# Performance work log

Hardware: AMD Instinct MI355X
Metric: run time of the kernel (lower is better)

## Reference

```python
import jax, jax.numpy as jnp
import numpy as np

N_NODES = 100000
N_EDGES = 3200000
N_FEAT = 128
EMBED = 20
N_CLASSES = 10
N_GRAPHS = 64


def setup_inputs() -> dict:
    key = jax.random.key(0)
    ks = jax.random.split(key, 8)
    x = jax.random.normal(ks[0], (N_NODES, N_FEAT), dtype=jnp.float32)
    edge_index = jax.random.randint(ks[1], (2, N_EDGES), 0, N_NODES, dtype=jnp.int64)
    edge_weights = jax.random.uniform(ks[2], (N_EDGES,), dtype=jnp.float32)
    batch = jnp.sort(jax.random.randint(ks[3], (N_NODES,), 0, N_GRAPHS, dtype=jnp.int64))
    # GCNConv parameters (glorot-ish scale) and final linear layer
    W = jax.random.normal(ks[4], (N_FEAT, EMBED), dtype=jnp.float32) * (1.0 / np.sqrt(N_FEAT))
    b = jnp.zeros((EMBED,), dtype=jnp.float32)
    lin_W = jax.random.normal(ks[5], (2 * EMBED, N_CLASSES), dtype=jnp.float32) * (1.0 / np.sqrt(2 * EMBED))
    lin_b = jnp.zeros((N_CLASSES,), dtype=jnp.float32)
    return {"x": x, "edge_index": edge_index, "edge_weights": edge_weights,
            "batch": batch, "W": W, "b": b, "lin_W": lin_W, "lin_b": lin_b}


def reference(x, edge_index, edge_weights, batch, W, b, lin_W, lin_b):
    N = x.shape[0]
    # --- GCNConv with self-loops and symmetric normalization (PyG semantics) ---
    loops = jnp.arange(N, dtype=edge_index.dtype)
    src = jnp.concatenate([edge_index[0], loops])
    dst = jnp.concatenate([edge_index[1], loops])
    w = jnp.concatenate([edge_weights, jnp.ones((N,), dtype=edge_weights.dtype)])
    deg = jax.ops.segment_sum(w, dst, num_segments=N)  # degree at targets
    dinv = jnp.where(deg > 0, jax.lax.rsqrt(deg), 0.0)
    norm = dinv[src] * w * dinv[dst]  # [E+N]
    xw = x @ W  # [N, EMBED]
    msg = xw[src] * norm[:, None]  # gather + scale
    out1 = jax.ops.segment_sum(msg, dst, num_segments=N) + b  # scatter-add
    # --- L2 normalize per node (F.normalize p=2 dim=1, eps=1e-12), then ReLU ---
    nrm = jnp.sqrt(jnp.sum(out1 * out1, axis=1, keepdims=True))
    embed = jax.nn.relu(out1 / jnp.maximum(nrm, 1e-12))
    # --- global max / mean pool per graph ---
    mx = jax.ops.segment_max(embed, batch, num_segments=N_GRAPHS)
    mx = jnp.where(jnp.isfinite(mx), mx, 0.0)  # empty graphs -> 0
    cnt = jax.ops.segment_sum(jnp.ones((N,), dtype=embed.dtype), batch, num_segments=N_GRAPHS)
    mean = jax.ops.segment_sum(embed, batch, num_segments=N_GRAPHS) / jnp.maximum(cnt, 1.0)[:, None]
    pooled = jnp.concatenate([mx, mean], axis=-1)  # [G, 2*EMBED]
    return pooled @ lin_W + lin_b
```

## Files before the change

### kernel.cpp

```cpp
#include <hip/hip_runtime.h>
#include <hip/hip_fp16.h>

#define NN 100000
#define NE 3200000
#define NF 128
#define EM 20
#define NC 10
#define NG 64

#define NB 782
#define CAPB 4608
#define T 4096
#define SBLK 1024

__global__ __launch_bounds__(SBLK) void k_scatter(
        const int* __restrict__ src, const int* __restrict__ dst,
        const float* __restrict__ w, int* __restrict__ gcursor,
        uint2* __restrict__ barr) {
    __shared__ unsigned int cnt[1024];
    __shared__ unsigned int off[1024];
    __shared__ unsigned int gbase[NB];
    __shared__ unsigned int wsum[16];
    __shared__ uint2 staged[T];
    __shared__ unsigned short bkt[T];
    int tid = threadIdx.x;
    long E0 = (long)blockIdx.x * T;
    int tot = (int)min((long)T, (long)NE - E0);
    cnt[tid] = 0;
    __syncthreads();
    unsigned int dreg[T / SBLK];
#pragma unroll
    for (int k = 0; k < T / SBLK; ++k) {
        int e = k * SBLK + tid;
        dreg[k] = 0;
        if (e < tot) {
            dreg[k] = (unsigned)dst[E0 + e];
            atomicAdd(&cnt[dreg[k] >> 7], 1u);
        }
    }
    __syncthreads();
    {
        int lane = tid & 63, wv = tid >> 6;
        unsigned int v = cnt[tid];
        unsigned int s = v;
#pragma unroll
        for (int o = 1; o < 64; o <<= 1) {
            unsigned int t = __shfl_up(s, o);
            if (lane >= o) s += t;
        }
        if (lane == 63) wsum[wv] = s;
        __syncthreads();
        if (tid == 0) {
            unsigned int a = 0;
#pragma unroll
            for (int i = 0; i < 16; ++i) { unsigned int t = wsum[i]; wsum[i] = a; a += t; }
        }
        __syncthreads();
        off[tid] = wsum[wv] + s - v;
    }
    __syncthreads();
    if (tid < NB) {
        unsigned int c = cnt[tid];
        gbase[tid] = c ? (unsigned int)atomicAdd(&gcursor[tid], (int)c) : 0u;
        cnt[tid] = 0;
    }
    __syncthreads();
#pragma unroll
    for (int k = 0; k < T / SBLK; ++k) {
        int e = k * SBLK + tid;
        if (e < tot) {
            long ge = E0 + e;
            unsigned int d = dreg[k];
            unsigned int b = d >> 7;
            unsigned int slot = atomicAdd(&cnt[b], 1u);
            unsigned int pos = off[b] + slot;
            staged[pos] = make_uint2((((unsigned)src[ge]) << 7) | (d & 127u),
                                     __float_as_uint(w[ge]));
            bkt[pos] = (unsigned short)b;
        }
    }
    __syncthreads();
    for (int i = tid; i < tot; i += SBLK) {
        unsigned int b = bkt[i];
        unsigned int gpos = gbase[b] + ((unsigned)i - off[b]);
        if (gpos < CAPB) barr[(size_t)b * CAPB + gpos] = staged[i];
    }
}

__global__ void k_degb(const int* __restrict__ gcursor, const uint2* __restrict__ barr,
                       float* __restrict__ dinv) {
    __shared__ float dacc[128];
    int bk = blockIdx.x, tid = threadIdx.x;
    if (tid < 128) dacc[tid] = 0.f;
    __syncthreads();
    int cntb = min(gcursor[bk], CAPB);
    const uint2* row = barr + (size_t)bk * CAPB;
    for (int i = tid; i < cntb; i += 1024) {
        uint2 r = row[i];
        atomicAdd(&dacc[r.x & 127u], __uint_as_float(r.y));
    }
    __syncthreads();
    if (tid < 128) {
        int gd = bk * 128 + tid;
        if (gd < NN) dinv[gd] = rsqrtf(1.0f + dacc[tid]);
    }
}

__global__ void k_xw(const float* __restrict__ x, const float* __restrict__ W,
                     const float* __restrict__ dinv,
                     __half* __restrict__ xwhA, __half* __restrict__ xwhB) {
    __shared__ float xs[64 * 129];
    __shared__ float Ws[NF * EM];
    int base = blockIdx.x * 64;
    for (int i = threadIdx.x; i < NF * EM; i += 256) Ws[i] = W[i];
    const float4* xg = (const float4*)(x + (size_t)base * NF);
    for (int v = threadIdx.x; v < 64 * NF / 4; v += 256) {
        int fidx = v * 4;
        size_t gidx = (size_t)base * NF + fidx;
        float4 val = (gidx + 3 < (size_t)NN * NF) ? xg[v] : make_float4(0.f, 0.f, 0.f, 0.f);
        int r = fidx / NF, c = fidx % NF;
        float* p = xs + r * 129 + c;
        p[0] = val.x; p[1] = val.y; p[2] = val.z; p[3] = val.w;
    }
    __syncthreads();
    int n = threadIdx.x & 63;
    int jg = threadIdx.x >> 6;
    int j0 = jg * 5;
    if (base + n >= NN) return;
    float acc[5] = {0.f, 0.f, 0.f, 0.f, 0.f};
    const float* xr = xs + n * 129;
#pragma unroll 4
    for (int k = 0; k < NF; ++k) {
        float xv = xr[k];
        const float* wr = Ws + k * EM + j0;
#pragma unroll
        for (int jj = 0; jj < 5; ++jj) acc[jj] = fmaf(xv, wr[jj], acc[jj]);
    }
    float dv = dinv[base + n];
#pragma unroll
    for (int jj = 0; jj < 5; ++jj) {
        int j = j0 + jj;
        __half hv = __float2half(acc[jj] * dv);
        if (j < 16) xwhA[(size_t)(base + n) * 16 + j] = hv;
        else        xwhB[(size_t)(base + n) * 4 + (j - 16)] = hv;
    }
}

__device__ inline void unpack16(uint4 a0, uint4 a1, float* f) {
    const __half2* h = (const __half2*)&a0;
#pragma unroll
    for (int c = 0; c < 4; ++c) { float2 t = __half22float2(h[c]); f[2*c] = t.x; f[2*c+1] = t.y; }
    h = (const __half2*)&a1;
#pragma unroll
    for (int c = 0; c < 4; ++c) { float2 t = __half22float2(h[c]); f[8+2*c] = t.x; f[9+2*c] = t.y; }
}
__device__ inline void unpack4(uint2 b0, float* f) {
    const __half2* h = (const __half2*)&b0;
#pragma unroll
    for (int c = 0; c < 2; ++c) { float2 t = __half22float2(h[c]); f[2*c] = t.x; f[2*c+1] = t.y; }
}

__global__ __launch_bounds__(1024, 8) void k_sortaggr(
                           const int* __restrict__ gcursor,
                           const unsigned long long* __restrict__ barr64,
                           const __half* __restrict__ xwhA, const __half* __restrict__ xwhB,
                           const float* __restrict__ dinv, const float* __restrict__ b,
                           float* __restrict__ embed) {
    __shared__ unsigned long long srt[CAPB];
    __shared__ unsigned int cnt[128];
    __shared__ unsigned int off[128];
    __shared__ unsigned int wtot;
    int bk = blockIdx.x, tid = threadIdx.x;
    if (tid < 128) cnt[tid] = 0;
    __syncthreads();
    int cntb = min(gcursor[bk], CAPB);
    const unsigned long long* row = barr64 + (size_t)bk * CAPB;
    unsigned long long rec[5];
    unsigned int pos[5];
    int K = 0;
    for (int e = tid; e < cntb; e += 1024) {
        rec[K] = row[e];
        pos[K] = atomicAdd(&cnt[(unsigned)rec[K] & 127u], 1u);
        ++K;
    }
    __syncthreads();
    unsigned int v = 0, s = 0;
    if (tid < 128) {
        v = cnt[tid]; s = v;
#pragma unroll
        for (int o = 1; o < 64; o <<= 1) {
            unsigned int t = __shfl_up(s, o);
            if ((tid & 63) >= o) s += t;
        }
        if (tid == 63) wtot = s;
    }
    __syncthreads();
    if (tid < 128) {
        if (tid >= 64) s += wtot;
        off[tid] = s;
    }
    __syncthreads();
    for (int k = 0; k < K; ++k) {
        unsigned int dl = (unsigned)rec[k] & 127u;
        srt[off[dl] - cnt[dl] + pos[k]] = rec[k];
    }
    __syncthreads();
    int d = tid >> 3, sub = tid & 7;
    int s0 = (int)(off[d] - cnt[d]), s1 = (int)off[d];
    const uint4* pA = (const uint4*)xwhA;
    const uint2* pB = (const uint2*)xwhB;
    float acc[20];
#pragma unroll
    for (int j = 0; j < 20; ++j) acc[j] = 0.f;
    for (int e = s0 + sub; e < s1; e += 8) {
        unsigned long long r = srt[e];
        unsigned int sN = ((unsigned int)r) >> 7;
        float nw = __uint_as_float((unsigned int)(r >> 32));
        uint4 a0 = pA[(size_t)sN * 2];
        uint4 a1 = pA[(size_t)sN * 2 + 1];
        uint2 b0 = pB[sN];
        const __half2* h0 = (const __half2*)&a0;
#pragma unroll
        for (int c = 0; c < 4; ++c) {
            float2 t = __half22float2(h0[c]);
            acc[2*c]   = fmaf(t.x, nw, acc[2*c]);
            acc[2*c+1] = fmaf(t.y, nw, acc[2*c+1]);
        }
        const __half2* h1 = (const __half2*)&a1;
#pragma unroll
        for (int c = 0; c < 4; ++c) {
            float2 t = __half22float2(h1[c]);
            acc[8+2*c]   = fmaf(t.x, nw, acc[8+2*c]);
            acc[9+2*c]   = fmaf(t.y, nw, acc[9+2*c]);
        }
        const __half2* h2 = (const __half2*)&b0;
#pragma unroll
        for (int c = 0; c < 2; ++c) {
            float2 t = __half22float2(h2[c]);
            acc[16+2*c] = fmaf(t.x, nw, acc[16+2*c]);
            acc[17+2*c] = fmaf(t.y, nw, acc[17+2*c]);
        }
    }
#pragma unroll
    for (int j = 0; j < 20; ++j) {
        acc[j] += __shfl_xor(acc[j], 1);
        acc[j] += __shfl_xor(acc[j], 2);
        acc[j] += __shfl_xor(acc[j], 4);
    }
    if (sub == 0) {
        int gd = bk * 128 + d;
        if (gd < NN) {
            float dv = dinv[gd];
            uint4 a0 = pA[(size_t)gd * 2];
            uint4 a1 = pA[(size_t)gd * 2 + 1];
            uint2 b0 = pB[gd];
            float xdh[20];
            unpack16(a0, a1, xdh);
            unpack4(b0, xdh + 16);
            float ss = 0.f;
#pragma unroll
            for (int j = 0; j < 20; ++j) {
                float r = fmaf(dv, acc[j] + xdh[j], b[j]);
                acc[j] = r;
                ss = fmaf(r, r, ss);
            }
            float inv = 1.0f / fmaxf(sqrtf(ss), 1e-12f);
            float4 o4[5];
            float* o = (float*)o4;
#pragma unroll
            for (int j = 0; j < 20; ++j) {
                float e2 = acc[j] * inv;
                o[j] = e2 > 0.f ? e2 : 0.f;
            }
            float4* eo = (float4*)(embed + (size_t)gd * EM);
#pragma unroll
            for (int c = 0; c < 5; ++c) eo[c] = o4[c];
        }
    }
}

__device__ inline int lbound(const int* __restrict__ batch, int key) {
    int lo = 0, hi = NN;
    while (lo < hi) {
        int mid = (lo + hi) >> 1;
        if (batch[mid] < key) lo = mid + 1; else hi = mid;
    }
    return lo;
}

__global__ void k_poolfinal(const float* __restrict__ embed, const int* __restrict__ batch,
                            const float* __restrict__ lw, const float* __restrict__ lb,
                            float* __restrict__ out) {
    __shared__ float cross[4][40];
    __shared__ float pooled[40];
    int g = blockIdx.x;
    int s0 = lbound(batch, g), s1 = lbound(batch, g + 1);
    int cnt = s1 - s0;
    float mx[EM], sm[EM];
#pragma unroll
    for (int j = 0; j < EM; ++j) { mx[j] = 0.f; sm[j] = 0.f; }
    for (int n = s0 + threadIdx.x; n < s1; n += 256) {
        const float4* e = (const float4*)(embed + (size_t)n * EM);
#pragma unroll
        for (int c = 0; c < 5; ++c) {
            float4 v = e[c];
            int j = c * 4;
            mx[j+0] = fmaxf(mx[j+0], v.x); sm[j+0] += v.x;
            mx[j+1] = fmaxf(mx[j+1], v.y); sm[j+1] += v.y;
            mx[j+2] = fmaxf(mx[j+2], v.z); sm[j+2] += v.z;
            mx[j+3] = fmaxf(mx[j+3], v.w); sm[j+3] += v.w;
        }
    }
#pragma unroll
    for (int o = 32; o > 0; o >>= 1) {
#pragma unroll
        for (int j = 0; j < EM; ++j) {
            mx[j] = fmaxf(mx[j], __shfl_xor(mx[j], o));
            sm[j] += __shfl_xor(sm[j], o);
        }
    }
    int wave = threadIdx.x >> 6, lane = threadIdx.x & 63;
    if (lane == 0) {
#pragma unroll
        for (int j = 0; j < EM; ++j) { cross[wave][j] = mx[j]; cross[wave][EM + j] = sm[j]; }
    }
    __syncthreads();
    if (threadIdx.x < 40) {
        int j = threadIdx.x;
        float v = cross[0][j];
        if (j < EM) v = fmaxf(fmaxf(v, cross[1][j]), fmaxf(cross[2][j], cross[3][j]));
        else        v = v + cross[1][j] + cross[2][j] + cross[3][j];
        if (j >= EM) v *= 1.0f / fmaxf((float)cnt, 1.0f);
        pooled[j] = v;
    }
    __syncthreads();
    if (threadIdx.x < NC) {
        int c = threadIdx.x;
        float acc = lb[c];
#pragma unroll
        for (int j = 0; j < 2 * EM; ++j) acc = fmaf(pooled[j], lw[j * NC + c], acc);
        out[g * NC + c] = acc;
    }
}

static inline size_t align_up(size_t v) { return (v + 1023) & ~(size_t)1023; }

extern "C" void kernel_launch(void* const* d_in, const int* in_sizes, int n_in,
                              void* d_out, int out_size, void* d_ws, size_t ws_size,
                              hipStream_t stream) {
    const float* x     = (const float*)d_in[0];
    const int*   ei    = (const int*)d_in[1];
    const float* ew    = (const float*)d_in[2];
    const int*   batch = (const int*)d_in[3];
    const float* W     = (const float*)d_in[4];
    const float* b     = (const float*)d_in[5];
    const float* lw    = (const float*)d_in[6];
    const float* lb    = (const float*)d_in[7];
    float* out = (float*)d_out;

    char* ws = (char*)d_ws;
    int*    gcursor = (int*)ws;    ws += align_up(4096);
    float*  dinv    = (float*)ws;  ws += align_up((size_t)NN * 4);
    __half* xwhA    = (__half*)ws; ws += align_up((size_t)NN * 16 * 2);
    __half* xwhB    = (__half*)ws; ws += align_up((size_t)NN * 4 * 2);
    float*  embed   = (float*)ws;  ws += align_up((size_t)NN * EM * 4);
    uint2*  barr    = (uint2*)ws;
    unsigned long long* barr64 = (unsigned long long*)barr;

    const int* srcp = ei;
    const int* dstp = ei + NE;

    (void)hipMemsetAsync(gcursor, 0, 4096, stream);
    k_scatter<<<(NE + T - 1) / T, SBLK, 0, stream>>>(srcp, dstp, ew, gcursor, barr);
    k_degb<<<NB, 1024, 0, stream>>>(gcursor, barr, dinv);
    k_xw<<<(NN + 63) / 64, 256, 0, stream>>>(x, W, dinv, xwhA, xwhB);
    k_sortaggr<<<NB, 1024, 0, stream>>>(gcursor, barr64, xwhA, xwhB, dinv, b, embed);
    k_poolfinal<<<NG, 256, 0, stream>>>(embed, batch, lw, lb, out);
}
```

Before: 276.1 us.

## Halve aggregation block size and software-pipeline neighbor gathers two deep

The sort-and-aggregate kernel now runs with 512 threads per block, giving each destination node 4 lanes instead of 8, so each thread holds up to 9 records. The edge loop is software-pipelined so the gathers for the next two edges are issued before the FMAs of the current one, keeping more memory requests in flight per thread. This targets gather latency in the aggregation step. In exchange there is more register pressure and less thread-level parallelism per block, and the out-of-range prefetch reads node 0 when a destination has fewer edges.

```diff
diff --git a/kernel.cpp b/kernel.cpp
--- a/kernel.cpp
+++ b/kernel.cpp
@@ -160,7 +160,31 @@
     for (int c = 0; c < 2; ++c) { float2 t = __half22float2(h[c]); f[2*c] = t.x; f[2*c+1] = t.y; }
 }
 
-__global__ __launch_bounds__(1024, 8) void k_sortaggr(
+__device__ inline void fma20(float* acc, uint4 a0, uint4 a1, uint2 b0, float nw) {
+    const __half2* h0 = (const __half2*)&a0;
+#pragma unroll
+    for (int c = 0; c < 4; ++c) {
+        float2 t = __half22float2(h0[c]);
+        acc[2*c]   = fmaf(t.x, nw, acc[2*c]);
+        acc[2*c+1] = fmaf(t.y, nw, acc[2*c+1]);
+    }
+    const __half2* h1 = (const __half2*)&a1;
+#pragma unroll
+    for (int c = 0; c < 4; ++c) {
+        float2 t = __half22float2(h1[c]);
+        acc[8+2*c] = fmaf(t.x, nw, acc[8+2*c]);
+        acc[9+2*c] = fmaf(t.y, nw, acc[9+2*c]);
+    }
+    const __half2* h2 = (const __half2*)&b0;
+#pragma unroll
+    for (int c = 0; c < 2; ++c) {
+        float2 t = __half22float2(h2[c]);
+        acc[16+2*c] = fmaf(t.x, nw, acc[16+2*c]);
+        acc[17+2*c] = fmaf(t.y, nw, acc[17+2*c]);
+    }
+}
+
+__global__ __launch_bounds__(512) void k_sortaggr(
                            const int* __restrict__ gcursor,
                            const unsigned long long* __restrict__ barr64,
                            const __half* __restrict__ xwhA, const __half* __restrict__ xwhB,
@@ -175,10 +199,10 @@
     __syncthreads();
     int cntb = min(gcursor[bk], CAPB);
     const unsigned long long* row = barr64 + (size_t)bk * CAPB;
-    unsigned long long rec[5];
-    unsigned int pos[5];
+    unsigned long long rec[9];
+    unsigned int pos[9];
     int K = 0;
-    for (int e = tid; e < cntb; e += 1024) {
+    for (int e = tid; e < cntb; e += 512) {
         rec[K] = row[e];
         pos[K] = atomicAdd(&cnt[(unsigned)rec[K] & 127u], 1u);
         ++K;
@@ -205,47 +229,47 @@
         srt[off[dl] - cnt[dl] + pos[k]] = rec[k];
     }
     __syncthreads();
-    int d = tid >> 3, sub = tid & 7;
+    int d = tid >> 2, sub = tid & 3;
     int s0 = (int)(off[d] - cnt[d]), s1 = (int)off[d];
     const uint4* pA = (const uint4*)xwhA;
     const uint2* pB = (const uint2*)xwhB;
     float acc[20];
 #pragma unroll
     for (int j = 0; j < 20; ++j) acc[j] = 0.f;
-    for (int e = s0 + sub; e < s1; e += 8) {
-        unsigned long long r = srt[e];
-        unsigned int sN = ((unsigned int)r) >> 7;
-        float nw = __uint_as_float((unsigned int)(r >> 32));
-        uint4 a0 = pA[(size_t)sN * 2];
-        uint4 a1 = pA[(size_t)sN * 2 + 1];
-        uint2 b0 = pB[sN];
-        const __half2* h0 = (const __half2*)&a0;
-#pragma unroll
-        for (int c = 0; c < 4; ++c) {
-            float2 t = __half22float2(h0[c]);
-            acc[2*c]   = fmaf(t.x, nw, acc[2*c]);
-            acc[2*c+1] = fmaf(t.y, nw, acc[2*c+1]);
-        }
-        const __half2* h1 = (const __half2*)&a1;
-#pragma unroll
-        for (int c = 0; c < 4; ++c) {
-            float2 t = __half22float2(h1[c]);
-            acc[8+2*c]   = fmaf(t.x, nw, acc[8+2*c]);
-            acc[9+2*c]   = fmaf(t.y, nw, acc[9+2*c]);
-        }
-        const __half2* h2 = (const __half2*)&b0;
-#pragma unroll
-        for (int c = 0; c < 2; ++c) {
-            float2 t = __half22float2(h2[c]);
-            acc[16+2*c] = fmaf(t.x, nw, acc[16+2*c]);
-            acc[17+2*c] = fmaf(t.y, nw, acc[17+2*c]);
-        }
+    int e0 = s0 + sub;
+    if (e0 < s1) {
+        unsigned long long rA = srt[e0];
+        unsigned int sA = ((unsigned int)rA) >> 7;
+        float nA = __uint_as_float((unsigned int)(rA >> 32));
+        uint4 A0 = pA[(size_t)sA * 2];
+        uint4 A1 = pA[(size_t)sA * 2 + 1];
+        uint2 A2 = pB[sA];
+        int eB = e0 + 4;
+        bool hB = eB < s1;
+        unsigned long long rB = hB ? srt[eB] : 0ULL;
+        unsigned int sB = ((unsigned int)rB) >> 7;
+        float nB = __uint_as_float((unsigned int)(rB >> 32));
+        uint4 B0 = pA[(size_t)sB * 2];
+        uint4 B1 = pA[(size_t)sB * 2 + 1];
+        uint2 B2 = pB[sB];
+        for (int ec = e0 + 8; ec < s1; ec += 4) {
+            unsigned long long rC = srt[ec];
+            unsigned int sC = ((unsigned int)rC) >> 7;
+            float nC = __uint_as_float((unsigned int)(rC >> 32));
+            uint4 C0 = pA[(size_t)sC * 2];
+            uint4 C1 = pA[(size_t)sC * 2 + 1];
+            uint2 C2 = pB[sC];
+            fma20(acc, A0, A1, A2, nA);
+            A0 = B0; A1 = B1; A2 = B2; nA = nB;
+            B0 = C0; B1 = C1; B2 = C2; nB = nC;
+        }
+        fma20(acc, A0, A1, A2, nA);
+        if (hB) fma20(acc, B0, B1, B2, nB);
     }
 #pragma unroll
     for (int j = 0; j < 20; ++j) {
         acc[j] += __shfl_xor(acc[j], 1);
         acc[j] += __shfl_xor(acc[j], 2);
-        acc[j] += __shfl_xor(acc[j], 4);
     }
     if (sub == 0) {
         int gd = bk * 128 + d;
@@ -374,6 +398,6 @@
     k_scatter<<<(NE + T - 1) / T, SBLK, 0, stream>>>(srcp, dstp, ew, gcursor, barr);
     k_degb<<<NB, 1024, 0, stream>>>(gcursor, barr, dinv);
     k_xw<<<(NN + 63) / 64, 256, 0, stream>>>(x, W, dinv, xwhA, xwhB);
-    k_sortaggr<<<NB, 1024, 0, stream>>>(gcursor, barr64, xwhA, xwhB, dinv, b, embed);
+    k_sortaggr<<<NB, 512, 0, stream>>>(gcursor, barr64, xwhA, xwhB, dinv, b, embed);
     k_poolfinal<<<NG, 256, 0, stream>>>(embed, batch, lw, lb, out);
 }
```

New measurement: 266.6 us. 3.4% less time.

## Fuse degree and fp16 projection scaling into aggregation kernel via grid barrier

Applied to the files above, without the earlier changes.

Removes the separate degree kernel and computes per-node degree inside the sort-aggregate kernel, which already reads each destination bucket, so the bucket array is no longer read twice. The node projection kernel now runs first and writes unscaled fp32 values; the fused kernel scales its own 128 nodes by the inverse square root of degree, writes the fp16 gather tables, then waits on a software grid-wide barrier (atomic counter plus spin) before gathering neighbours. Block size drops to 512 threads with 4 lanes per destination node, and the embed buffer now aliases the fp32 projection buffer. The barrier is only safe if all 782 blocks are resident at once, which carries deadlock risk, and the extra fp32 write and read adds memory traffic.

```diff
diff --git a/kernel.cpp b/kernel.cpp
--- a/kernel.cpp
+++ b/kernel.cpp
@@ -87,28 +87,8 @@
     }
 }
 
-__global__ void k_degb(const int* __restrict__ gcursor, const uint2* __restrict__ barr,
-                       float* __restrict__ dinv) {
-    __shared__ float dacc[128];
-    int bk = blockIdx.x, tid = threadIdx.x;
-    if (tid < 128) dacc[tid] = 0.f;
-    __syncthreads();
-    int cntb = min(gcursor[bk], CAPB);
-    const uint2* row = barr + (size_t)bk * CAPB;
-    for (int i = tid; i < cntb; i += 1024) {
-        uint2 r = row[i];
-        atomicAdd(&dacc[r.x & 127u], __uint_as_float(r.y));
-    }
-    __syncthreads();
-    if (tid < 128) {
-        int gd = bk * 128 + tid;
-        if (gd < NN) dinv[gd] = rsqrtf(1.0f + dacc[tid]);
-    }
-}
-
 __global__ void k_xw(const float* __restrict__ x, const float* __restrict__ W,
-                     const float* __restrict__ dinv,
-                     __half* __restrict__ xwhA, __half* __restrict__ xwhB) {
+                     float* __restrict__ xwf) {
     __shared__ float xs[64 * 129];
     __shared__ float Ws[NF * EM];
     int base = blockIdx.x * 64;
@@ -136,14 +116,9 @@
 #pragma unroll
         for (int jj = 0; jj < 5; ++jj) acc[jj] = fmaf(xv, wr[jj], acc[jj]);
     }
-    float dv = dinv[base + n];
-#pragma unroll
-    for (int jj = 0; jj < 5; ++jj) {
-        int j = j0 + jj;
-        __half hv = __float2half(acc[jj] * dv);
-        if (j < 16) xwhA[(size_t)(base + n) * 16 + j] = hv;
-        else        xwhB[(size_t)(base + n) * 4 + (j - 16)] = hv;
-    }
+#pragma unroll
+    for (int jj = 0; jj < 5; ++jj)
+        xwf[(size_t)(base + n) * EM + j0 + jj] = acc[jj];
 }
 
 __device__ inline void unpack16(uint4 a0, uint4 a1, float* f) {
@@ -160,27 +135,55 @@
     for (int c = 0; c < 2; ++c) { float2 t = __half22float2(h[c]); f[2*c] = t.x; f[2*c+1] = t.y; }
 }
 
-__global__ __launch_bounds__(1024, 8) void k_sortaggr(
-                           const int* __restrict__ gcursor,
+__device__ inline void fma20(float* acc, uint4 a0, uint4 a1, uint2 b0, float nw) {
+    const __half2* h0 = (const __half2*)&a0;
+#pragma unroll
+    for (int c = 0; c < 4; ++c) {
+        float2 t = __half22float2(h0[c]);
+        acc[2*c]   = fmaf(t.x, nw, acc[2*c]);
+        acc[2*c+1] = fmaf(t.y, nw, acc[2*c+1]);
+    }
+    const __half2* h1 = (const __half2*)&a1;
+#pragma unroll
+    for (int c = 0; c < 4; ++c) {
+        float2 t = __half22float2(h1[c]);
+        acc[8+2*c] = fmaf(t.x, nw, acc[8+2*c]);
+        acc[9+2*c] = fmaf(t.y, nw, acc[9+2*c]);
+    }
+    const __half2* h2 = (const __half2*)&b0;
+#pragma unroll
+    for (int c = 0; c < 2; ++c) {
+        float2 t = __half22float2(h2[c]);
+        acc[16+2*c] = fmaf(t.x, nw, acc[16+2*c]);
+        acc[17+2*c] = fmaf(t.y, nw, acc[17+2*c]);
+    }
+}
+
+__global__ __launch_bounds__(512, 8) void k_fused(
+                           const int* __restrict__ gcursor, int* bar,
                            const unsigned long long* __restrict__ barr64,
-                           const __half* __restrict__ xwhA, const __half* __restrict__ xwhB,
-                           const float* __restrict__ dinv, const float* __restrict__ b,
-                           float* __restrict__ embed) {
+                           const float* xwf,
+                           __half* __restrict__ xwhA, __half* __restrict__ xwhB,
+                           const float* __restrict__ b, float* embed) {
     __shared__ unsigned long long srt[CAPB];
     __shared__ unsigned int cnt[128];
     __shared__ unsigned int off[128];
+    __shared__ float dacc[128];
+    __shared__ float dvs[128];
     __shared__ unsigned int wtot;
     int bk = blockIdx.x, tid = threadIdx.x;
-    if (tid < 128) cnt[tid] = 0;
+    if (tid < 128) { cnt[tid] = 0; dacc[tid] = 0.f; }
     __syncthreads();
     int cntb = min(gcursor[bk], CAPB);
     const unsigned long long* row = barr64 + (size_t)bk * CAPB;
-    unsigned long long rec[5];
-    unsigned int pos[5];
+    unsigned long long rec[9];
+    unsigned int pos[9];
     int K = 0;
-    for (int e = tid; e < cntb; e += 1024) {
+    for (int e = tid; e < cntb; e += 512) {
         rec[K] = row[e];
-        pos[K] = atomicAdd(&cnt[(unsigned)rec[K] & 127u], 1u);
+        unsigned int dl = (unsigned)rec[K] & 127u;
+        pos[K] = atomicAdd(&cnt[dl], 1u);
+        atomicAdd(&dacc[dl], __uint_as_float((unsigned)(rec[K] >> 32)));
         ++K;
     }
     __syncthreads();
@@ -198,59 +201,54 @@
     if (tid < 128) {
         if (tid >= 64) s += wtot;
         off[tid] = s;
+        dvs[tid] = rsqrtf(1.0f + dacc[tid]);
     }
     __syncthreads();
     for (int k = 0; k < K; ++k) {
         unsigned int dl = (unsigned)rec[k] & 127u;
         srt[off[dl] - cnt[dl] + pos[k]] = rec[k];
     }
-    __syncthreads();
-    int d = tid >> 3, sub = tid & 7;
+    for (int i = tid; i < 128 * EM; i += 512) {
+        int node = i / EM, dim = i - node * EM;
+        int gd = bk * 128 + node;
+        if (gd < NN) {
+            __half hv = __float2half(xwf[(size_t)gd * EM + dim] * dvs[node]);
+            if (dim < 16) xwhA[(size_t)gd * 16 + dim] = hv;
+            else          xwhB[(size_t)gd * 4 + (dim - 16)] = hv;
+        }
+    }
+    __syncthreads();
+    if (tid == 0) {
+        __hip_atomic_fetch_add(bar, 1, __ATOMIC_ACQ_REL, __HIP_MEMORY_SCOPE_AGENT);
+        while (__hip_atomic_load(bar, __ATOMIC_ACQUIRE, __HIP_MEMORY_SCOPE_AGENT) < NB)
+            __builtin_amdgcn_s_sleep(2);
+    }
+    __syncthreads();
+    int d = tid >> 2, sub = tid & 3;
     int s0 = (int)(off[d] - cnt[d]), s1 = (int)off[d];
     const uint4* pA = (const uint4*)xwhA;
     const uint2* pB = (const uint2*)xwhB;
     float acc[20];
 #pragma unroll
     for (int j = 0; j < 20; ++j) acc[j] = 0.f;
-    for (int e = s0 + sub; e < s1; e += 8) {
+    for (int e = s0 + sub; e < s1; e += 4) {
         unsigned long long r = srt[e];
         unsigned int sN = ((unsigned int)r) >> 7;
         float nw = __uint_as_float((unsigned int)(r >> 32));
         uint4 a0 = pA[(size_t)sN * 2];
         uint4 a1 = pA[(size_t)sN * 2 + 1];
         uint2 b0 = pB[sN];
-        const __half2* h0 = (const __half2*)&a0;
-#pragma unroll
-        for (int c = 0; c < 4; ++c) {
-            float2 t = __half22float2(h0[c]);
-            acc[2*c]   = fmaf(t.x, nw, acc[2*c]);
-            acc[2*c+1] = fmaf(t.y, nw, acc[2*c+1]);
-        }
-        const __half2* h1 = (const __half2*)&a1;
-#pragma unroll
-        for (int c = 0; c < 4; ++c) {
-            float2 t = __half22float2(h1[c]);
-            acc[8+2*c]   = fmaf(t.x, nw, acc[8+2*c]);
-            acc[9+2*c]   = fmaf(t.y, nw, acc[9+2*c]);
-        }
-        const __half2* h2 = (const __half2*)&b0;
-#pragma unroll
-        for (int c = 0; c < 2; ++c) {
-            float2 t = __half22float2(h2[c]);
-            acc[16+2*c] = fmaf(t.x, nw, acc[16+2*c]);
-            acc[17+2*c] = fmaf(t.y, nw, acc[17+2*c]);
-        }
+        fma20(acc, a0, a1, b0, nw);
     }
 #pragma unroll
     for (int j = 0; j < 20; ++j) {
         acc[j] += __shfl_xor(acc[j], 1);
         acc[j] += __shfl_xor(acc[j], 2);
-        acc[j] += __shfl_xor(acc[j], 4);
     }
     if (sub == 0) {
         int gd = bk * 128 + d;
         if (gd < NN) {
-            float dv = dinv[gd];
+            float dv = dvs[d];
             uint4 a0 = pA[(size_t)gd * 2];
             uint4 a1 = pA[(size_t)gd * 2 + 1];
             uint2 b0 = pB[gd];
@@ -360,20 +358,20 @@
 
     char* ws = (char*)d_ws;
     int*    gcursor = (int*)ws;    ws += align_up(4096);
-    float*  dinv    = (float*)ws;  ws += align_up((size_t)NN * 4);
+    float*  xwf     = (float*)ws;  ws += align_up((size_t)NN * EM * 4);
     __half* xwhA    = (__half*)ws; ws += align_up((size_t)NN * 16 * 2);
     __half* xwhB    = (__half*)ws; ws += align_up((size_t)NN * 4 * 2);
-    float*  embed   = (float*)ws;  ws += align_up((size_t)NN * EM * 4);
     uint2*  barr    = (uint2*)ws;
     unsigned long long* barr64 = (unsigned long long*)barr;
+    float*  embed   = xwf;
+    int*    bar     = gcursor + 1000;
 
     const int* srcp = ei;
     const int* dstp = ei + NE;
 
     (void)hipMemsetAsync(gcursor, 0, 4096, stream);
+    k_xw<<<(NN + 63) / 64, 256, 0, stream>>>(x, W, xwf);
     k_scatter<<<(NE + T - 1) / T, SBLK, 0, stream>>>(srcp, dstp, ew, gcursor, barr);
-    k_degb<<<NB, 1024, 0, stream>>>(gcursor, barr, dinv);
-    k_xw<<<(NN + 63) / 64, 256, 0, stream>>>(x, W, dinv, xwhA, xwhB);
-    k_sortaggr<<<NB, 1024, 0, stream>>>(gcursor, barr64, xwhA, xwhB, dinv, b, embed);
+    k_fused<<<NB, 512, 0, stream>>>(gcursor, bar, barr64, xwf, xwhA, xwhB, b, embed);
     k_poolfinal<<<NG, 256, 0, stream>>>(embed, batch, lw, lb, out);
 }
```

Result: slower. 385.6 us (+39.6%).
